# Kernel optimization log

Hardware: AMD Instinct MI355X
Metric: run time of the kernel (lower is better)

Reference implementation:

```python
import jax, jax.numpy as jnp
import numpy as np

# Model dims
N_ENT = 128      # max_entities
E_DIM = 768      # entity_dim
D_EMB = 768      # embedding_dim
HEADS = 12
KEY_DIM = E_DIM // HEADS  # 64
STEPS = 3
DENSITY = 0.8
THRESH = 0.001
MAX_SEQ = 1024


def setup_inputs() -> dict:
    key = jax.random.key(0)
    ks = jax.random.split(key, 20)
    B, S = 4, 1024

    def glorot(k, shape, fan_in, fan_out):
        std = np.sqrt(2.0 / (fan_in + fan_out)).astype(np.float32)
        return jax.random.normal(k, shape, dtype=jnp.float32) * std

    inp = {}
    inp['embeddings'] = jax.random.normal(ks[0], (B, S, D_EMB), dtype=jnp.float32)
    inp['graph_init'] = jax.random.uniform(ks[1], (B, N_ENT, N_ENT), dtype=jnp.float32)
    # learnable entity library (glorot_normal)
    inp['entity_library'] = glorot(ks[2], (N_ENT, E_DIM), N_ENT, E_DIM)
    # positional embedding table
    inp['pos_table'] = jax.random.normal(ks[3], (MAX_SEQ, D_EMB), dtype=jnp.float32) * 0.02
    # MultiHeadAttention projections (keras-style per-head)
    inp['Wq'] = glorot(ks[4], (E_DIM, HEADS, KEY_DIM), E_DIM, HEADS * KEY_DIM)
    inp['bq'] = jnp.zeros((HEADS, KEY_DIM), jnp.float32)
    inp['Wk'] = glorot(ks[5], (D_EMB, HEADS, KEY_DIM), D_EMB, HEADS * KEY_DIM)
    inp['bk'] = jnp.zeros((HEADS, KEY_DIM), jnp.float32)
    inp['Wv'] = glorot(ks[6], (D_EMB, HEADS, KEY_DIM), D_EMB, HEADS * KEY_DIM)
    inp['bv'] = jnp.zeros((HEADS, KEY_DIM), jnp.float32)
    inp['Wo'] = glorot(ks[7], (HEADS, KEY_DIM, E_DIM), HEADS * KEY_DIM, E_DIM)
    inp['bo'] = jnp.zeros((E_DIM,), jnp.float32)
    # refinement MLP: (2E + 1 + D) -> E (gelu) -> 1 (tanh)
    rin = 2 * E_DIM + 1 + D_EMB
    inp['W1'] = glorot(ks[8], (rin, E_DIM), rin, E_DIM)
    inp['b1'] = jnp.zeros((E_DIM,), jnp.float32)
    inp['W2'] = glorot(ks[9], (E_DIM, 1), E_DIM, 1)
    inp['b2'] = jnp.zeros((1,), jnp.float32)
    # sparsification gate: 2E -> E (gelu) -> 1 (sigmoid)
    inp['Wg1'] = glorot(ks[10], (2 * E_DIM, E_DIM), 2 * E_DIM, E_DIM)
    inp['bg1'] = jnp.zeros((E_DIM,), jnp.float32)
    inp['Wg2'] = glorot(ks[11], (E_DIM, 1), E_DIM, 1)
    inp['bg2'] = jnp.zeros((1,), jnp.float32)
    return inp


def reference(embeddings, graph_init, entity_library, pos_table,
              Wq, bq, Wk, bk, Wv, bv, Wo, bo,
              W1, b1, W2, b2, Wg1, bg1, Wg2, bg2):
    B, S, D = embeddings.shape
    N, E = entity_library.shape

    # positional encoding
    x = embeddings + pos_table[:S][None]  # (B,S,D)

    # --- entity extraction: MHA(query=entity_library, key=value=x) ---
    q = jnp.einsum('ne,ehk->nhk', entity_library, Wq) + bq          # (N,H,K)
    k = jnp.einsum('bsd,dhk->bshk', x, Wk) + bk                     # (B,S,H,K)
    v = jnp.einsum('bsd,dhk->bshk', x, Wv) + bv                     # (B,S,H,K)
    scores = jnp.einsum('nhk,bshk->bhns', q, k) / jnp.sqrt(
        jnp.asarray(KEY_DIM, x.dtype))                              # (B,H,N,S)
    attn = jax.nn.softmax(scores, axis=-1)
    ctx = jnp.einsum('bhns,bshk->bnhk', attn, v)                    # (B,N,H,K)
    entities = jnp.einsum('bnhk,hke->bne', ctx, Wo) + bo            # (B,N,E)

    # entity activity: max over heads and key positions
    activity = jnp.max(attn, axis=(1, 3))                           # (B,N)
    entity_mask = (activity > THRESH).astype(jnp.float32)           # (B,N)

    # global context: mean over sequence
    context = jnp.mean(x, axis=1)                                   # (B,D)

    # initial dense graph: uniform(-density, density)
    graph = graph_init * (2.0 * DENSITY) - DENSITY                  # (B,N,N)

    # pairwise edge features (B,N,N,2E)
    ei = jnp.broadcast_to(entities[:, :, None, :], (B, N, N, E))
    ej = jnp.broadcast_to(entities[:, None, :, :], (B, N, N, E))
    edge_feat = jnp.concatenate([ei, ej], axis=-1)
    ctx_tiled = jnp.broadcast_to(context[:, None, None, :], (B, N, N, D))

    # iterative refinement: concat -> MLP(gelu) -> tanh update, residual add
    for _ in range(STEPS):
        ref_in = jnp.concatenate(
            [edge_feat, graph[..., None], ctx_tiled], axis=-1)      # (B,N,N,2E+1+D)
        h = jax.nn.gelu(jnp.einsum('bijf,fe->bije', ref_in, W1) + b1)
        upd = jnp.tanh(jnp.einsum('bije,eo->bijo', h, W2) + b2)[..., 0]
        graph = graph + upd

    # sparsification gate on edge features
    gh = jax.nn.gelu(jnp.einsum('bijf,fe->bije', edge_feat, Wg1) + bg1)
    gate = jax.nn.sigmoid(jnp.einsum('bije,eo->bijo', gh, Wg2) + bg2)[..., 0]
    graph = graph * gate

    # mask inactive entities
    graph = graph * entity_mask[:, :, None] * entity_mask[:, None, :]
    entities = entities * entity_mask[..., None]
    return entities, graph, entity_mask
```

## Files before the change

kernel.cpp:

```cpp
#include <hip/hip_runtime.h>
#include <hip/hip_bf16.h>
#include <math.h>

namespace {
constexpr int SEQ  = 1024;
constexpr int NE   = 128;

typedef float f32x4  __attribute__((ext_vector_type(4)));
typedef short bf16x8 __attribute__((ext_vector_type(8)));

__device__ __forceinline__ float rcp_fast(float x) {
  return __builtin_amdgcn_rcpf(x);
}

__device__ __forceinline__ float gelu_fast(float x) {
  float x2 = x * x;
  float t = fmaf(x2, -0.1029443f, -2.3022093f);
  return x * rcp_fast(1.0f + exp2f(x * t));
}

__device__ __forceinline__ float tanh_fast(float x) {
  return 1.0f - 2.0f * rcp_fast(1.0f + exp2f(x * 2.8853901f));
}

__device__ __forceinline__ float sigmoid_fast(float x) {
  return rcp_fast(1.0f + exp2f(x * -1.4426950f));
}

__device__ __forceinline__ ushort f2bf(float f) {
  union { float f; unsigned u; } c; c.f = f;
  unsigned u = c.u;
  u += 0x7FFF + ((u >> 16) & 1);
  return (ushort)(u >> 16);
}

__global__ __launch_bounds__(256) void posadd_bf16_kernel(
    const float* __restrict__ emb, const float* __restrict__ pos,
    ushort* __restrict__ xb) {
  int i = blockIdx.x * 256 + threadIdx.x;
  const int perB = SEQ * 768 / 8;
  int pi = i - (i / perB) * perB;
  float4 e0 = ((const float4*)emb)[i * 2];
  float4 e1 = ((const float4*)emb)[i * 2 + 1];
  float4 p0 = ((const float4*)pos)[pi * 2];
  float4 p1 = ((const float4*)pos)[pi * 2 + 1];
  ushort o[8];
  o[0] = f2bf(e0.x + p0.x); o[1] = f2bf(e0.y + p0.y);
  o[2] = f2bf(e0.z + p0.z); o[3] = f2bf(e0.w + p0.w);
  o[4] = f2bf(e1.x + p1.x); o[5] = f2bf(e1.y + p1.y);
  o[6] = f2bf(e1.z + p1.z); o[7] = f2bf(e1.w + p1.w);
  *(uint4*)&xb[(size_t)i * 8] = *(uint4*)o;
}

__global__ __launch_bounds__(256) void wconv_kernel(
    const float* __restrict__ Wk, const float* __restrict__ Wv,
    ushort* __restrict__ WtK, ushort* __restrict__ WtV) {
  const float* __restrict__ W  = blockIdx.z ? Wv : Wk;
  ushort* __restrict__ Wt = blockIdx.z ? WtV : WtK;
  const int k0 = blockIdx.x * 64, n0 = blockIdx.y * 64;
  __shared__ ushort sT[64][72];
  const int t = threadIdx.x;
  const int rr = t >> 4, c4 = (t & 15) * 4;
#pragma unroll
  for (int i = 0; i < 4; ++i) {
    int r = rr + 16 * i;
    float4 v = *(const float4*)&W[(size_t)(k0 + r) * 768 + n0 + c4];
    sT[c4 + 0][r] = f2bf(v.x);
    sT[c4 + 1][r] = f2bf(v.y);
    sT[c4 + 2][r] = f2bf(v.z);
    sT[c4 + 3][r] = f2bf(v.w);
  }
  __syncthreads();
#pragma unroll
  for (int j = 0; j < 2; ++j) {
    int cid = t + 256 * j;
    int nr = cid >> 3, kc8 = (cid & 7) * 8;
    *(uint4*)&Wt[(size_t)(n0 + nr) * 768 + k0 + kc8] = *(uint4*)&sT[nr][kc8];
  }
}

__global__ __launch_bounds__(256) void ctxmean_kernel(
    const float* __restrict__ emb, const float* __restrict__ pos,
    float* __restrict__ ctxv) {
  int b = blockIdx.x / 12, chunk = blockIdx.x % 12;
  int lane = threadIdx.x & 63, sg = threadIdx.x >> 6;
  int d = chunk * 64 + lane;
  float acc = 0.f;
  const float* eb = emb + ((size_t)b * SEQ + sg) * 768 + d;
  const float* pp = pos + (size_t)sg * 768 + d;
  for (int s = sg; s < SEQ; s += 4) {
    acc += *eb + *pp;
    eb += 4 * 768; pp += 4 * 768;
  }
  __shared__ float red[4][64];
  red[sg][lane] = acc;
  __syncthreads();
  if (threadIdx.x < 64) {
    float t = red[0][threadIdx.x] + red[1][threadIdx.x] +
              red[2][threadIdx.x] + red[3][threadIdx.x];
    ctxv[b * 768 + chunk * 64 + threadIdx.x] = t * (1.0f / 1024.0f);
  }
}

__global__ __launch_bounds__(256) void gemm768_kernel(
    const float* __restrict__ A, const float* __restrict__ W,
    const float* __restrict__ bias, float* __restrict__ C, int M) {
  __shared__ __align__(16) float sA[16][68];
  __shared__ __align__(16) float sB[16][68];
  const int bm = blockIdx.x * 64;
  const int bn = blockIdx.y * 64;
  const int tid = threadIdx.x;
  const int tm = (tid >> 4) * 4;
  const int tn = (tid & 15) * 4;
  const int lm = tid >> 2, lkq = (tid & 3) * 4;
  const int lkk = tid >> 4, lnq = (tid & 15) * 4;
  float acc[4][4] = {};
  for (int k0 = 0; k0 < 768; k0 += 16) {
    float4 av = make_float4(0.f, 0.f, 0.f, 0.f);
    if (bm + lm < M) av = *(const float4*)&A[(size_t)(bm + lm) * 768 + k0 + lkq];
    float4 wv = *(const float4*)&W[(size_t)(k0 + lkk) * 768 + bn + lnq];
    __syncthreads();
    sA[lkq + 0][lm] = av.x; sA[lkq + 1][lm] = av.y;
    sA[lkq + 2][lm] = av.z; sA[lkq + 3][lm] = av.w;
    *(float4*)&sB[lkk][lnq] = wv;
    __syncthreads();
#pragma unroll
    for (int kk = 0; kk < 16; ++kk) {
      float4 a = *(const float4*)&sA[kk][tm];
      float4 w = *(const float4*)&sB[kk][tn];
      acc[0][0] += a.x * w.x; acc[0][1] += a.x * w.y; acc[0][2] += a.x * w.z; acc[0][3] += a.x * w.w;
      acc[1][0] += a.y * w.x; acc[1][1] += a.y * w.y; acc[1][2] += a.y * w.z; acc[1][3] += a.y * w.w;
      acc[2][0] += a.z * w.x; acc[2][1] += a.z * w.y; acc[2][2] += a.z * w.z; acc[2][3] += a.z * w.w;
      acc[3][0] += a.w * w.x; acc[3][1] += a.w * w.y; acc[3][2] += a.w * w.z; acc[3][3] += a.w * w.w;
    }
  }
#pragma unroll
  for (int i = 0; i < 4; ++i) {
    int row = bm + tm + i;
    if (row < M) {
#pragma unroll
      for (int j = 0; j < 4; ++j) {
        float o = acc[i][j];
        if (bias) o += bias[bn + tn + j];
        C[(size_t)row * 768 + bn + tn + j] = o;
      }
    }
  }
}

struct ProjParams {
  const float* W[4];
  const float* bias[4];
  float* C[4];
};

__global__ __launch_bounds__(256) void gemm768x4_kernel(
    const float* __restrict__ A, ProjParams pp) {
  __shared__ __align__(16) float sA[16][68];
  __shared__ __align__(16) float sB[16][68];
  const int sel = blockIdx.y / 12;
  const float* W = pp.W[sel];
  const float* bias = pp.bias[sel];
  float* C = pp.C[sel];
  const int bm = blockIdx.x * 64;
  const int bn = (blockIdx.y % 12) * 64;
  const int tid = threadIdx.x;
  const int tm = (tid >> 4) * 4;
  const int tn = (tid & 15) * 4;
  const int lm = tid >> 2, lkq = (tid & 3) * 4;
  const int lkk = tid >> 4, lnq = (tid & 15) * 4;
  float acc[4][4] = {};
  for (int k0 = 0; k0 < 768; k0 += 16) {
    float4 av = *(const float4*)&A[(size_t)(bm + lm) * 768 + k0 + lkq];
    float4 wv = *(const float4*)&W[(size_t)(k0 + lkk) * 768 + bn + lnq];
    __syncthreads();
    sA[lkq + 0][lm] = av.x; sA[lkq + 1][lm] = av.y;
    sA[lkq + 2][lm] = av.z; sA[lkq + 3][lm] = av.w;
    *(float4*)&sB[lkk][lnq] = wv;
    __syncthreads();
#pragma unroll
    for (int kk = 0; kk < 16; ++kk) {
      float4 a = *(const float4*)&sA[kk][tm];
      float4 w = *(const float4*)&sB[kk][tn];
      acc[0][0] += a.x * w.x; acc[0][1] += a.x * w.y; acc[0][2] += a.x * w.z; acc[0][3] += a.x * w.w;
      acc[1][0] += a.y * w.x; acc[1][1] += a.y * w.y; acc[1][2] += a.y * w.z; acc[1][3] += a.y * w.w;
      acc[2][0] += a.z * w.x; acc[2][1] += a.z * w.y; acc[2][2] += a.z * w.z; acc[2][3] += a.z * w.w;
      acc[3][0] += a.w * w.x; acc[3][1] += a.w * w.y; acc[3][2] += a.w * w.z; acc[3][3] += a.w * w.w;
    }
  }
#pragma unroll
  for (int i = 0; i < 4; ++i) {
    int row = bm + tm + i;
#pragma unroll
    for (int j = 0; j < 4; ++j) {
      float o = acc[i][j];
      if (bias) o += bias[bn + tn + j];
      C[(size_t)row * 768 + bn + tn + j] = o;
    }
  }
}

__global__ __launch_bounds__(256) void kv_mfma_kernel(
    const ushort* __restrict__ xb,
    const ushort* __restrict__ WtK,
    const ushort* __restrict__ WtV,
    const float* __restrict__ bk, const float* __restrict__ bv,
    float* __restrict__ k2, float* __restrict__ v2) {
  __shared__ ushort sA[64][40];
  __shared__ ushort sBt[128][40];
  const int bm = blockIdx.x * 64;
  const bool isV = blockIdx.y >= 6;
  const int bn = (blockIdx.y % 6) * 128;
  const ushort* __restrict__ Wt = isV ? WtV : WtK;
  const float* __restrict__ bias = isV ? bv : bk;
  float* __restrict__ out = isV ? v2 : k2;
  const int t = threadIdx.x;
  const int ar = t >> 2, ac8 = (t & 3) * 8;
  const int wr = t >> 2, wc8 = (t & 3) * 8;

  const ushort* __restrict__ Axp = xb + (size_t)(bm + ar) * 768 + ac8;
  const ushort* __restrict__ Wp0 = Wt + (size_t)(bn + wr) * 768 + wc8;
  const ushort* __restrict__ Wp1 = Wt + (size_t)(bn + wr + 64) * 768 + wc8;

  uint4 ra  = *(const uint4*)(Axp);
  uint4 rw0 = *(const uint4*)(Wp0);
  uint4 rw1 = *(const uint4*)(Wp1);

  const int lane = t & 63;
  const int w = t >> 6;
  const int lrow = lane & 15;
  const int lk8 = (lane >> 4) * 8;

  f32x4 acc[8] = {};
  for (int k0 = 0; k0 < 768; k0 += 32) {
    __syncthreads();
    *(uint4*)&sA[ar][ac8] = ra;
    *(uint4*)&sBt[wr][wc8] = rw0;
    *(uint4*)&sBt[wr + 64][wc8] = rw1;
    __syncthreads();
    if (k0 + 32 < 768) {
      ra  = *(const uint4*)(Axp + k0 + 32);
      rw0 = *(const uint4*)(Wp0 + k0 + 32);
      rw1 = *(const uint4*)(Wp1 + k0 + 32);
    }
    bf16x8 a = *(const bf16x8*)&sA[w * 16 + lrow][lk8];
#pragma unroll
    for (int nf = 0; nf < 8; ++nf) {
      bf16x8 b = *(const bf16x8*)&sBt[nf * 16 + lrow][lk8];
      acc[nf] = __builtin_amdgcn_mfma_f32_16x16x32_bf16(a, b, acc[nf], 0, 0, 0);
    }
  }

  const int bidx = bm >> 10;
  const int s_base = bm & 1023;
  const int h0 = bn >> 6;
  const int rg = (lane >> 4) * 4;
#pragma unroll
  for (int nf = 0; nf < 8; ++nf) {
    int nl = nf * 16 + lrow;
    int h = h0 + (nl >> 6);
    int c = nl & 63;
    float bsv = bias[bn + nl];
    float* op = out + (((size_t)(bidx * 12 + h)) * 1024 + s_base + w * 16 + rg) * 64 + c;
#pragma unroll
    for (int r = 0; r < 4; ++r)
      op[(size_t)r * 64] = acc[nf][r] + bsv;
  }
}

__global__ __launch_bounds__(256) void attn2_kernel(
    const float* __restrict__ q, const float* __restrict__ k2,
    const float* __restrict__ v2, float* __restrict__ ctx,
    float* __restrict__ invsum) {
  __shared__ float p[16][1028];
  __shared__ float4 sK[128 * 16];
  __shared__ float4 sQ[16][16];
  __shared__ float linv[16];
  __shared__ float4 part[4][4][4][16];

  const int xcd = blockIdx.x & 7;
  const int slot = blockIdx.x >> 3;
  const int bh = xcd * 6 + (slot >> 3);
  const int ng = slot & 7;
  const int b = bh / 12, h = bh % 12;
  const int t = threadIdx.x;

  {
    int nn = t >> 4, dq = t & 15;
    float4 qv = *(const float4*)&q[(size_t)(ng * 16 + nn) * 768 + h * 64 + dq * 4];
    qv.x *= 0.125f; qv.y *= 0.125f; qv.z *= 0.125f; qv.w *= 0.125f;
    sQ[nn][dq] = qv;
  }
  const float4* kbh = (const float4*)(k2 + ((size_t)(b * 12 + h)) * 1024 * 64);
  const float4* vbh = (const float4*)(v2 + ((size_t)(b * 12 + h)) * 1024 * 64);

  const int npair = t >> 5;
  const int g = t & 31;
  const int n0 = npair * 2, n1 = n0 + 1;

  for (int c = 0; c < 8; ++c) {
    __syncthreads();
#pragma unroll
    for (int w = 0; w < 8; ++w) {
      int fi = w * 256 + t;
      int sl = fi >> 4, dq = fi & 15;
      sK[sl * 16 + (dq ^ (sl & 7))] = kbh[c * 2048 + fi];
    }
    __syncthreads();
    float4 a0[4] = {}, a1[4] = {};
#pragma unroll
    for (int d0 = 0; d0 < 16; ++d0) {
      float4 q0 = sQ[n0][d0];
      float4 q1 = sQ[n1][d0];
      int slot2 = d0 ^ (g & 7);
#pragma unroll
      for (int u = 0; u < 4; ++u) {
        float4 kv = sK[(g + 32 * u) * 16 + slot2];
        a0[u].x += q0.x * kv.x; a0[u].y += q0.y * kv.y;
        a0[u].z += q0.z * kv.z; a0[u].w += q0.w * kv.w;
        a1[u].x += q1.x * kv.x; a1[u].y += q1.y * kv.y;
        a1[u].z += q1.z * kv.z; a1[u].w += q1.w * kv.w;
      }
    }
#pragma unroll
    for (int u = 0; u < 4; ++u) {
      int s = c * 128 + g + 32 * u;
      p[n0][s] = a0[u].x + a0[u].y + a0[u].z + a0[u].w;
      p[n1][s] = a1[u].x + a1[u].y + a1[u].z + a1[u].w;
    }
  }
  __syncthreads();

  {
    int n = t >> 4, sub = t & 15;
    float m = -1e30f;
#pragma unroll 8
    for (int u = 0; u < 64; ++u) m = fmaxf(m, p[n][sub + 16 * u]);
    m = fmaxf(m, __shfl_xor(m, 1)); m = fmaxf(m, __shfl_xor(m, 2));
    m = fmaxf(m, __shfl_xor(m, 4)); m = fmaxf(m, __shfl_xor(m, 8));
    float sum = 0.f;
#pragma unroll 8
    for (int u = 0; u < 64; ++u) {
      float e = __expf(p[n][sub + 16 * u] - m);
      p[n][sub + 16 * u] = e;
      sum += e;
    }
    sum += __shfl_xor(sum, 1); sum += __shfl_xor(sum, 2);
    sum += __shfl_xor(sum, 4); sum += __shfl_xor(sum, 8);
    if (sub == 0) {
      float inv = 1.0f / sum;
      linv[n] = inv;
      invsum[(b * 12 + h) * 128 + ng * 16 + n] = inv;
    }
  }

  const int dq = t & 15, nq = (t >> 4) & 3, sq = t >> 6;
  float4 acc[4] = {};
  for (int c = 0; c < 8; ++c) {
    __syncthreads();
#pragma unroll
    for (int w = 0; w < 8; ++w) {
      int fi = w * 256 + t;
      int sl = fi >> 4, dqq = fi & 15;
      sK[sl * 16 + (dqq ^ (sl & 7))] = vbh[c * 2048 + fi];
    }
    __syncthreads();
#pragma unroll 2
    for (int v4 = 0; v4 < 32; v4 += 4) {
      int sl0 = sq * 32 + v4;
      int s0 = c * 128 + sl0;
      float pr[4][4];
#pragma unroll
      for (int i = 0; i < 4; ++i)
        *(float4*)&pr[i][0] = *(const float4*)&p[nq * 4 + i][s0];
#pragma unroll
      for (int u = 0; u < 4; ++u) {
        int sl = sl0 + u;
        float4 vv = sK[sl * 16 + (dq ^ (sl & 7))];
#pragma unroll
        for (int i = 0; i < 4; ++i) {
          float pw = pr[i][u];
          acc[i].x += pw * vv.x; acc[i].y += pw * vv.y;
          acc[i].z += pw * vv.z; acc[i].w += pw * vv.w;
        }
      }
    }
  }
#pragma unroll
  for (int i = 0; i < 4; ++i) part[sq][nq][i][dq] = acc[i];
  __syncthreads();
  {
    int n = t >> 4, dqq = t & 15;
    float4 r0 = part[0][n >> 2][n & 3][dqq];
    float4 r1 = part[1][n >> 2][n & 3][dqq];
    float4 r2 = part[2][n >> 2][n & 3][dqq];
    float4 r3 = part[3][n >> 2][n & 3][dqq];
    float inv = linv[n];
    float4 o;
    o.x = (r0.x + r1.x + r2.x + r3.x) * inv;
    o.y = (r0.y + r1.y + r2.y + r3.y) * inv;
    o.z = (r0.z + r1.z + r2.z + r3.z) * inv;
    o.w = (r0.w + r1.w + r2.w + r3.w) * inv;
    *(float4*)&ctx[(size_t)(b * 128 + ng * 16 + n) * 768 + h * 64 + dqq * 4] = o;
  }
}

__global__ void mask_kernel(const float* __restrict__ invsum,
                            float* __restrict__ mask_out) {
  int t = threadIdx.x;
  int b = t >> 7, n = t & 127;
  float a = 0.f;
  for (int h = 0; h < 12; ++h) a = fmaxf(a, invsum[(b * 12 + h) * 128 + n]);
  mask_out[t] = (a > 0.001f) ? 1.0f : 0.0f;
}

__global__ __launch_bounds__(256) void entmask_kernel(
    const float* __restrict__ ent, const float* __restrict__ mask,
    float* __restrict__ out) {
  int bi = blockIdx.x;
  float m = mask[bi];
  for (int e = threadIdx.x; e < 768; e += 256)
    out[(size_t)bi * 768 + e] = ent[(size_t)bi * 768 + e] * m;
}

__global__ __launch_bounds__(256) void refine_kernel(
    const float* __restrict__ A1, const float* __restrict__ B1,
    const float* __restrict__ C1, const float* __restrict__ w1g,
    const float* __restrict__ W2, const float* __restrict__ b2,
    const float* __restrict__ Ag, const float* __restrict__ Bg,
    const float* __restrict__ Wg2, const float* __restrict__ bg2,
    const float* __restrict__ graph_init, const float* __restrict__ mask,
    float* __restrict__ graph_out) {
  const int bi = blockIdx.x >> 2;
  const int jq = blockIdx.x & 3;
  const int b = bi >> 7;
  const int lane = threadIdx.x & 63, wv = threadIdx.x >> 6;

  float base[12], w1gr[12], w2r[12], agr[12], wg2r[12];
#pragma unroll
  for (int r = 0; r < 12; ++r) {
    int e = r * 64 + lane;
    base[r] = A1[(size_t)bi * 768 + e] + C1[b * 768 + e];
    w1gr[r] = w1g[e];
    w2r[r]  = W2[e];
    agr[r]  = Ag[(size_t)bi * 768 + e];
    wg2r[r] = Wg2[e];
  }
  const float b2s = b2[0], bg2s = bg2[0];
  const float mi = mask[bi];

  const int jend = jq * 32 + 32;
  for (int j = jq * 32 + wv; j < jend; j += 4) {
    float g = graph_init[(size_t)bi * 128 + j] * 1.6f - 0.8f;
    const float* B1j = &B1[((size_t)(b * NE + j)) * 768 + lane];
    const float* Bgj = &Bg[((size_t)(b * NE + j)) * 768 + lane];
    float pre[12], gpre[12];
#pragma unroll
    for (int r = 0; r < 12; ++r) {
      pre[r]  = base[r] + B1j[r * 64];
      gpre[r] = agr[r] + Bgj[r * 64];
    }
#pragma unroll
    for (int st = 0; st < 3; ++st) {
      float acc = 0.f;
#pragma unroll
      for (int r = 0; r < 12; ++r) {
        float hx = pre[r] + g * w1gr[r];
        acc += gelu_fast(hx) * w2r[r];
      }
      acc += __shfl_xor(acc, 1);  acc += __shfl_xor(acc, 2);
      acc += __shfl_xor(acc, 4);  acc += __shfl_xor(acc, 8);
      acc += __shfl_xor(acc, 16); acc += __shfl_xor(acc, 32);
      g += tanh_fast(acc + b2s);
    }
    float gacc = 0.f;
#pragma unroll
    for (int r = 0; r < 12; ++r) gacc += gelu_fast(gpre[r]) * wg2r[r];
    gacc += __shfl_xor(gacc, 1);  gacc += __shfl_xor(gacc, 2);
    gacc += __shfl_xor(gacc, 4);  gacc += __shfl_xor(gacc, 8);
    gacc += __shfl_xor(gacc, 16); gacc += __shfl_xor(gacc, 32);
    float gate = sigmoid_fast(gacc + bg2s);
    if (lane == 0)
      graph_out[(size_t)bi * 128 + j] = g * gate * mi * mask[b * NE + j];
  }
}

}

extern "C" void kernel_launch(void* const* d_in, const int* in_sizes, int n_in,
                              void* d_out, int out_size, void* d_ws, size_t ws_size,
                              hipStream_t stream) {
  const float* emb  = (const float*)d_in[0];
  const float* ginit= (const float*)d_in[1];
  const float* lib  = (const float*)d_in[2];
  const float* pos  = (const float*)d_in[3];
  const float* Wq   = (const float*)d_in[4];
  const float* bq   = (const float*)d_in[5];
  const float* Wk   = (const float*)d_in[6];
  const float* bk   = (const float*)d_in[7];
  const float* Wv   = (const float*)d_in[8];
  const float* bv   = (const float*)d_in[9];
  const float* Wo   = (const float*)d_in[10];
  const float* bo   = (const float*)d_in[11];
  const float* W1   = (const float*)d_in[12];
  const float* b1   = (const float*)d_in[13];
  const float* W2   = (const float*)d_in[14];
  const float* b2   = (const float*)d_in[15];
  const float* Wg1  = (const float*)d_in[16];
  const float* bg1  = (const float*)d_in[17];
  const float* Wg2  = (const float*)d_in[18];
  const float* bg2  = (const float*)d_in[19];

  float* ws = (float*)d_ws;
  float* k2   = ws + 0;
  float* v2   = ws + 3145728;
  ushort* xb  = (ushort*)(ws + 6291456);
  float* A1   = ws + 6291456;
  float* B1   = ws + 6684672;
  float* Ag   = ws + 7077888;
  float* Bg   = ws + 7471104;
  ushort* WtK = (ushort*)(ws + 7864320);
  ushort* WtV = WtK + 589824;
  float* q_   = ws + 9437184;
  float* ctx_ = ws + 9535488;
  float* ent_ = ws + 9928704;
  float* ctxv = ws + 10321920;
  float* C1   = ws + 10324992;
  float* invs = ws + 10328064;

  float* out_ent   = (float*)d_out;
  float* out_graph = out_ent + 393216;
  float* out_mask  = out_ent + 458752;

  wconv_kernel<<<dim3(12, 12, 2), 256, 0, stream>>>(Wk, Wv, WtK, WtV);
  posadd_bf16_kernel<<<1536, 256, 0, stream>>>(emb, pos, xb);
  ctxmean_kernel<<<48, 256, 0, stream>>>(emb, pos, ctxv);
  gemm768_kernel<<<dim3(2, 12), 256, 0, stream>>>(lib, Wq, bq, q_, 128);
  kv_mfma_kernel<<<dim3(64, 12), 256, 0, stream>>>(xb, WtK, WtV, bk, bv, k2, v2);
  attn2_kernel<<<384, 256, 0, stream>>>(q_, k2, v2, ctx_, invs);
  mask_kernel<<<1, 512, 0, stream>>>(invs, out_mask);
  gemm768_kernel<<<dim3(8, 12), 256, 0, stream>>>(ctx_, Wo, bo, ent_, 512);
  entmask_kernel<<<512, 256, 0, stream>>>(ent_, out_mask, out_ent);
  ProjParams pp;
  pp.W[0] = W1;              pp.bias[0] = nullptr; pp.C[0] = A1;
  pp.W[1] = W1 + 589824;     pp.bias[1] = nullptr; pp.C[1] = B1;
  pp.W[2] = Wg1;             pp.bias[2] = bg1;     pp.C[2] = Ag;
  pp.W[3] = Wg1 + 589824;    pp.bias[3] = nullptr; pp.C[3] = Bg;
  gemm768x4_kernel<<<dim3(8, 48), 256, 0, stream>>>(ent_, pp);
  gemm768_kernel<<<dim3(1, 12), 256, 0, stream>>>(ctxv, W1 + 1537 * 768, b1, C1, 4);
  refine_kernel<<<2048, 256, 0, stream>>>(A1, B1, C1, W1 + 1536 * 768, W2, b2,
                                          Ag, Bg, Wg2, bg2, ginit, out_mask,
                                          out_graph);
}
```

Before: 618.1 us.

## Fuse attention into single pass with online softmax and register prefetch of K/V

```diff
diff --git a/kernel.cpp b/kernel.cpp
--- a/kernel.cpp
+++ b/kernel.cpp
@@ -272,11 +272,11 @@
     const float* __restrict__ q, const float* __restrict__ k2,
     const float* __restrict__ v2, float* __restrict__ ctx,
     float* __restrict__ invsum) {
-  __shared__ float p[16][1028];
-  __shared__ float4 sK[128 * 16];
+  __shared__ float4 sK[2048];
+  __shared__ float p[16][144];
   __shared__ float4 sQ[16][16];
+  __shared__ float frow[16];
   __shared__ float linv[16];
-  __shared__ float4 part[4][4][4][16];
 
   const int xcd = blockIdx.x & 7;
   const int slot = blockIdx.x >> 3;
@@ -294,25 +294,37 @@
   const float4* kbh = (const float4*)(k2 + ((size_t)(b * 12 + h)) * 1024 * 64);
   const float4* vbh = (const float4*)(v2 + ((size_t)(b * 12 + h)) * 1024 * 64);
 
-  const int npair = t >> 5;
-  const int g = t & 31;
+  const int g = t & 31, npair = t >> 5;
   const int n0 = npair * 2, n1 = n0 + 1;
+  const int rn = t >> 4, sub = t & 15;
+  const int dq = t & 15, nq = (t >> 4) & 3, sq = t >> 6;
+
+  float m_run = -1e30f, sum_run = 0.f;
+  float4 acc[4] = {};
+  float4 kreg[8], vreg[8];
+
+#pragma unroll
+  for (int w = 0; w < 8; ++w) kreg[w] = kbh[w * 256 + t];
 
   for (int c = 0; c < 8; ++c) {
     __syncthreads();
 #pragma unroll
     for (int w = 0; w < 8; ++w) {
       int fi = w * 256 + t;
-      int sl = fi >> 4, dq = fi & 15;
-      sK[sl * 16 + (dq ^ (sl & 7))] = kbh[c * 2048 + fi];
-    }
-    __syncthreads();
+      int sl = fi >> 4, dd = fi & 15;
+      sK[sl * 16 + (dd ^ (sl & 15))] = kreg[w];
+    }
+    __syncthreads();
+#pragma unroll
+    for (int w = 0; w < 8; ++w)
+      vreg[w] = vbh[c * 2048 + w * 256 + t];
+
     float4 a0[4] = {}, a1[4] = {};
 #pragma unroll
     for (int d0 = 0; d0 < 16; ++d0) {
       float4 q0 = sQ[n0][d0];
       float4 q1 = sQ[n1][d0];
-      int slot2 = d0 ^ (g & 7);
+      int slot2 = d0 ^ (g & 15);
 #pragma unroll
       for (int u = 0; u < 4; ++u) {
         float4 kv = sK[(g + 32 * u) * 16 + slot2];
@@ -324,59 +336,62 @@
     }
 #pragma unroll
     for (int u = 0; u < 4; ++u) {
-      int s = c * 128 + g + 32 * u;
+      int s = g + 32 * u;
       p[n0][s] = a0[u].x + a0[u].y + a0[u].z + a0[u].w;
       p[n1][s] = a1[u].x + a1[u].y + a1[u].z + a1[u].w;
     }
-  }
-  __syncthreads();
-
-  {
-    int n = t >> 4, sub = t & 15;
-    float m = -1e30f;
-#pragma unroll 8
-    for (int u = 0; u < 64; ++u) m = fmaxf(m, p[n][sub + 16 * u]);
-    m = fmaxf(m, __shfl_xor(m, 1)); m = fmaxf(m, __shfl_xor(m, 2));
-    m = fmaxf(m, __shfl_xor(m, 4)); m = fmaxf(m, __shfl_xor(m, 8));
-    float sum = 0.f;
-#pragma unroll 8
-    for (int u = 0; u < 64; ++u) {
-      float e = __expf(p[n][sub + 16 * u] - m);
-      p[n][sub + 16 * u] = e;
-      sum += e;
-    }
-    sum += __shfl_xor(sum, 1); sum += __shfl_xor(sum, 2);
-    sum += __shfl_xor(sum, 4); sum += __shfl_xor(sum, 8);
-    if (sub == 0) {
-      float inv = 1.0f / sum;
-      linv[n] = inv;
-      invsum[(b * 12 + h) * 128 + ng * 16 + n] = inv;
-    }
-  }
-
-  const int dq = t & 15, nq = (t >> 4) & 3, sq = t >> 6;
-  float4 acc[4] = {};
-  for (int c = 0; c < 8; ++c) {
-    __syncthreads();
+    __syncthreads();
+
+    float cm = -1e30f;
+#pragma unroll
+    for (int u = 0; u < 8; ++u) cm = fmaxf(cm, p[rn][sub + 16 * u]);
+    cm = fmaxf(cm, __shfl_xor(cm, 1)); cm = fmaxf(cm, __shfl_xor(cm, 2));
+    cm = fmaxf(cm, __shfl_xor(cm, 4)); cm = fmaxf(cm, __shfl_xor(cm, 8));
+    float mn = fmaxf(m_run, cm);
+    float f = __expf(m_run - mn);
+    float csum = 0.f;
+#pragma unroll
+    for (int u = 0; u < 8; ++u) {
+      float e = __expf(p[rn][sub + 16 * u] - mn);
+      p[rn][sub + 16 * u] = e;
+      csum += e;
+    }
+    csum += __shfl_xor(csum, 1); csum += __shfl_xor(csum, 2);
+    csum += __shfl_xor(csum, 4); csum += __shfl_xor(csum, 8);
+    sum_run = sum_run * f + csum;
+    m_run = mn;
+    if (sub == 0) frow[rn] = f;
+
 #pragma unroll
     for (int w = 0; w < 8; ++w) {
       int fi = w * 256 + t;
-      int sl = fi >> 4, dqq = fi & 15;
-      sK[sl * 16 + (dqq ^ (sl & 7))] = vbh[c * 2048 + fi];
-    }
-    __syncthreads();
+      int sl = fi >> 4, dd = fi & 15;
+      sK[sl * 16 + (dd ^ (sl & 15))] = vreg[w];
+    }
+    __syncthreads();
+
+    if (c < 7) {
+#pragma unroll
+      for (int w = 0; w < 8; ++w)
+        kreg[w] = kbh[(c + 1) * 2048 + w * 256 + t];
+    }
+
+#pragma unroll
+    for (int i = 0; i < 4; ++i) {
+      float fr = frow[nq * 4 + i];
+      acc[i].x *= fr; acc[i].y *= fr; acc[i].z *= fr; acc[i].w *= fr;
+    }
 #pragma unroll 2
     for (int v4 = 0; v4 < 32; v4 += 4) {
       int sl0 = sq * 32 + v4;
-      int s0 = c * 128 + sl0;
       float pr[4][4];
 #pragma unroll
       for (int i = 0; i < 4; ++i)
-        *(float4*)&pr[i][0] = *(const float4*)&p[nq * 4 + i][s0];
+        *(float4*)&pr[i][0] = *(const float4*)&p[nq * 4 + i][sl0];
 #pragma unroll
       for (int u = 0; u < 4; ++u) {
         int sl = sl0 + u;
-        float4 vv = sK[sl * 16 + (dq ^ (sl & 7))];
+        float4 vv = sK[sl * 16 + (dq ^ (sl & 15))];
 #pragma unroll
         for (int i = 0; i < 4; ++i) {
           float pw = pr[i][u];
@@ -386,15 +401,23 @@
       }
     }
   }
-#pragma unroll
-  for (int i = 0; i < 4; ++i) part[sq][nq][i][dq] = acc[i];
+
+  if (sub == 0) {
+    float inv = 1.0f / sum_run;
+    linv[rn] = inv;
+    invsum[(b * 12 + h) * 128 + ng * 16 + rn] = inv;
+  }
+  __syncthreads();
+#pragma unroll
+  for (int i = 0; i < 4; ++i)
+    sK[((sq * 4 + nq) * 4 + i) * 16 + dq] = acc[i];
   __syncthreads();
   {
     int n = t >> 4, dqq = t & 15;
-    float4 r0 = part[0][n >> 2][n & 3][dqq];
-    float4 r1 = part[1][n >> 2][n & 3][dqq];
-    float4 r2 = part[2][n >> 2][n & 3][dqq];
-    float4 r3 = part[3][n >> 2][n & 3][dqq];
+    float4 r0 = sK[((0 * 4 + (n >> 2)) * 4 + (n & 3)) * 16 + dqq];
+    float4 r1 = sK[((1 * 4 + (n >> 2)) * 4 + (n & 3)) * 16 + dqq];
+    float4 r2 = sK[((2 * 4 + (n >> 2)) * 4 + (n & 3)) * 16 + dqq];
+    float4 r3 = sK[((3 * 4 + (n >> 2)) * 4 + (n & 3)) * 16 + dqq];
     float inv = linv[n];
     float4 o;
     o.x = (r0.x + r1.x + r2.x + r3.x) * inv;
```

After: 615.4 us. About the same (-0.4%).
